# Kernel optimization log

Hardware: AMD Instinct MI355X
Metric: run time of the kernel (lower is better)

## Reference

```python
import jax, jax.numpy as jnp
import numpy as np

N, E, C, NB, NE, G = 20000, 320000, 64, 8, 4, 16
L2 = 9          # (max_ell+1)^2 with max_ell=2
RMAX = 5.0
HID = 16        # nonlinear readout hidden width


def setup_inputs():
    key = jax.random.key(0)
    ks = jax.random.split(key, 16)
    positions = jax.random.uniform(ks[0], (N, 3), dtype=jnp.float32) * 3.0
    elems = jax.random.randint(ks[1], (N,), 0, NE)
    node_attrs = jax.nn.one_hot(elems, NE, dtype=jnp.float32)
    edge_index = jax.random.randint(ks[2], (2, E), 0, N)
    batch = jnp.sort(jax.random.randint(ks[3], (N,), 0, G))
    shifts = jnp.zeros((E, 3), jnp.float32)
    atomic_energies = jnp.array([-1.0, -2.0, -3.0, -4.0], jnp.float32)
    sc = lambda k, shp, fan: jax.random.normal(k, shp, jnp.float32) / np.sqrt(fan).astype(np.float32)
    W_embed = sc(ks[4], (NE, C), NE)
    W_up = sc(ks[5], (2, C, C), C)
    W1 = sc(ks[6], (2, NB, 64), NB)
    W2 = sc(ks[7], (2, 64, C), 64)
    W_out = sc(ks[8], (2, C, C), C)
    W_skip = sc(ks[9], (2, NE, C), NE)
    w_read0 = sc(ks[10], (C,), C)
    W_r1 = sc(ks[11], (C, HID), C)
    w_r2 = sc(ks[12], (HID,), HID)
    return dict(positions=positions, node_attrs=node_attrs, shifts=shifts,
                atomic_energies=atomic_energies, W_embed=W_embed, W_up=W_up,
                W1=W1, W2=W2, W_out=W_out, W_skip=W_skip, w_read0=w_read0,
                W_r1=W_r1, w_r2=w_r2, edge_index=edge_index, batch=batch)


def _sph_harm_l2(u):
    # component-normalized real spherical harmonics up to l=2 on unit vectors
    x, y, z = u[:, 0], u[:, 1], u[:, 2]
    s3, s5, s15 = jnp.sqrt(3.0), jnp.sqrt(5.0), jnp.sqrt(15.0)
    return jnp.stack([jnp.ones_like(x),
                      s3 * x, s3 * y, s3 * z,
                      s15 * x * y, s15 * y * z, 0.5 * s5 * (3.0 * z * z - 1.0),
                      s15 * x * z, 0.5 * s15 * (x * x - y * y)], axis=-1)


def _radial(r):
    # Bessel radial basis with polynomial cutoff (p=6)
    n = jnp.arange(1, NB + 1, dtype=jnp.float32)
    rb = jnp.sqrt(2.0 / RMAX) * jnp.sin(n * jnp.pi * r[:, None] / RMAX) / r[:, None]
    u = r / RMAX
    fc = 1.0 - 28.0 * u**6 + 48.0 * u**7 - 21.0 * u**8
    fc = jnp.where(u < 1.0, fc, 0.0)
    return rb * fc[:, None]


def _energy_contributions(positions, node_attrs, shifts, atomic_energies,
                          W_embed, W_up, W1, W2, W_out, W_skip,
                          w_read0, W_r1, w_r2, edge_index, batch):
    snd, rcv = edge_index[0], edge_index[1]
    vec = positions[snd] - positions[rcv] + shifts                  # [E,3]
    r = jnp.sqrt(jnp.sum(vec * vec, axis=-1) + 1e-12)               # [E]
    Y = _sph_harm_l2(vec / r[:, None])                              # [E,L2]
    ef = _radial(r)                                                 # [E,NB]
    # E0: per-element reference energies, summed per graph
    e0 = jax.ops.segment_sum(node_attrs @ atomic_energies, batch, num_segments=G)
    h0 = node_attrs @ W_embed                                       # [N,C] scalar feats
    h = jnp.zeros((positions.shape[0], L2, C), h0.dtype).at[:, 0, :].set(h0)
    readouts = [lambda s: s @ w_read0,
                lambda s: jax.nn.silu(s @ W_r1) @ w_r2]             # linear / nonlinear
    energies = [e0]
    for i in range(2):
        hu = jnp.einsum('nlc,cd->nld', h, W_up[i])                  # channel mix
        R = jax.nn.silu(ef @ W1[i]) @ W2[i]                         # radial MLP [E,C]
        s = jnp.einsum('elc,el->ec', hu[snd], Y)                    # equivariant contraction
        m = Y[:, :, None] * (R * s)[:, None, :]                     # [E,L2,C] messages
        agg = jax.ops.segment_sum(m, rcv, num_segments=positions.shape[0])
        h = jnp.einsum('nlc,cd->nld', agg, W_out[i])
        h = h.at[:, 0, :].add(node_attrs @ W_skip[i])               # scalar skip connection
        node_en = readouts[i](h[:, 0, :])                           # [N]
        energies.append(jax.ops.segment_sum(node_en, batch, num_segments=G))
    return jnp.stack(energies, axis=-1)                             # [G, num_interactions+1]


def reference(positions, node_attrs, shifts, atomic_energies, W_embed, W_up,
              W1, W2, W_out, W_skip, w_read0, W_r1, w_r2, edge_index, batch):
    contributions = _energy_contributions(positions, node_attrs, shifts,
        atomic_energies, W_embed, W_up, W1, W2, W_out, W_skip,
        w_read0, W_r1, w_r2, edge_index, batch)
    total_energy = jnp.sum(contributions, axis=-1)                  # [G]
    forces = -jax.grad(lambda p: jnp.sum(_energy_contributions(p, node_attrs,
        shifts, atomic_energies, W_embed, W_up, W1, W2, W_out, W_skip,
        w_read0, W_r1, w_r2, edge_index, batch)))(positions)        # [N,3]
    return total_energy, contributions, forces
```

## Files before the change

### kernel.cpp

```cpp
#include <hip/hip_runtime.h>
#include <cmath>

constexpr int N_  = 20000;
constexpr int E_  = 320000;
constexpr int NE_ = 4;
constexpr int G_  = 16;
constexpr int CAP = 96;
constexpr int TAB = 4096;
constexpr float RMAXF = 5.0f;
constexpr float PI_F  = 3.14159265358979323846f;
constexpr float S3  = 1.7320508075688772f;
constexpr float S5  = 2.2360679774997896f;
constexpr float S15 = 3.8729833462074170f;
constexpr float KC_ = 0.6324555320336759f;

typedef unsigned short u16;
typedef unsigned int   u32;
typedef _Float16 f16;
typedef _Float16 f16x2 __attribute__((ext_vector_type(2)));

#define DEV static __device__ __forceinline__

__device__ float g_fallback[110000000];

DEV float sigmoidf_(float x){ return 1.0f/(1.0f+__expf(-x)); }

DEV float b2f(u16 u){ return __uint_as_float(((u32)u)<<16); }
DEV u16  f2b(float f){
  u32 x = __float_as_uint(f);
  return (u16)((x + 0x7FFFu + ((x>>16)&1u)) >> 16);
}
DEV u16  f2h(float f){ union{f16 h; u16 u;} v; v.h=(f16)f; return v.u; }
DEV float h2f(u16 u){ union{u16 u2; f16 h;} v; v.u2=u; return (float)v.h; }

DEV f16x2 u2h(u32 x){ union{u32 u; f16x2 h;} v; v.u=x; return v.h; }
DEV u32 h2u(f16x2 h){ union{u32 u; f16x2 h;} v; v.h=h; return v.u; }
DEV u32 pkh(float a, float b){ f16x2 h; h.x=(f16)a; h.y=(f16)b; return h2u(h); }

DEV void ld4(const float* __restrict__ p, float* d){
  float4 a = ((const float4*)p)[0];
  d[0]=a.x; d[1]=a.y; d[2]=a.z; d[3]=a.w;
}
DEV void ld4b(const u16* __restrict__ p, float* d){
  ushort4 a = *(const ushort4*)p;
  d[0]=b2f(a.x); d[1]=b2f(a.y); d[2]=b2f(a.z); d[3]=b2f(a.w);
}
DEV void st8h(u16* p, const float* d){
  uint4 v;
  v.x = pkh(d[0],d[1]); v.y = pkh(d[2],d[3]);
  v.z = pkh(d[4],d[5]); v.w = pkh(d[6],d[7]);
  *(uint4*)p = v;
}

DEV float tlerp(const u16* __restrict__ tab, int i0, float f, int idx){
  return h2f(tab[i0*256+idx])*(1.0f-f) + h2f(tab[(i0+1)*256+idx])*f;
}

__global__ void k_cnt(const int* __restrict__ ei, int* __restrict__ cntR){
  int e = blockIdx.x*256 + threadIdx.x;
  atomicAdd(&cntR[ei[E_+e]], 1);
}

__global__ void k_scan(const int* __restrict__ cntR, int* __restrict__ offR){
  __shared__ int part[256];
  int t = threadIdx.x;
  constexpr int CH = (N_+255)/256;
  int base = t*CH;
  int s=0;
  for (int i=0;i<CH;++i){ int idx=base+i; if(idx<N_) s+=cntR[idx]; }
  part[t]=s; __syncthreads();
  for (int d=1; d<256; d<<=1){
    int v = (t>=d)? part[t-d] : 0;
    __syncthreads();
    part[t]+=v;
    __syncthreads();
  }
  int run = (t==0)?0:part[t-1];
  for (int i=0;i<CH;++i){ int idx=base+i; if(idx<N_){ offR[idx]=run; run+=cntR[idx]; } }
  if (t==255) offR[N_]=run;
}

__global__ void k_perm(const int* __restrict__ ei, const int* __restrict__ offR,
                       int* __restrict__ cntR2, int* __restrict__ cntS,
                       int* __restrict__ pe, int* __restrict__ pSnd, int* __restrict__ pRcv,
                       int* __restrict__ listS){
  int e = blockIdx.x*256 + threadIdx.x;
  int s = ei[e], r = ei[E_+e];
  int p = offR[r] + atomicAdd(&cntR2[r], 1);
  pe[p] = e; pSnd[p] = s; pRcv[p] = r;
  int q = atomicAdd(&cntS[s], 1); if (q < CAP) listS[s*CAP+q] = p;
}

__global__ void k_pre(const float* __restrict__ Wout0, const float* __restrict__ Wup1,
                      const float* __restrict__ Wskip0, const float* __restrict__ wread0,
                      float* __restrict__ WA, float* __restrict__ sa,
                      float* __restrict__ va, float* __restrict__ sv){
  int t = threadIdx.x;
  for (int idx=t; idx<4096; idx+=256){
    int c = idx>>6, d = idx&63;
    float acc=0.f;
    for (int m=0;m<64;++m) acc += Wout0[c*64+m]*Wup1[m*64+d];
    WA[idx]=acc;
  }
  {
    int k = t>>6, d = t&63;
    float acc=0.f;
    for (int m=0;m<64;++m) acc += Wskip0[k*64+m]*Wup1[m*64+d];
    sa[t]=acc;
  }
  if (t<64){
    float acc=0.f;
    for (int d=0;d<64;++d) acc += Wout0[t*64+d]*wread0[d];
    va[t]=acc;
  }
  if (t<4){
    float acc=0.f;
    for (int d=0;d<64;++d) acc += Wskip0[t*64+d]*wread0[d];
    sv[t]=acc;
  }
}

__global__ __launch_bounds__(256, 2)
void k_rtab(const float* __restrict__ W1g, const float* __restrict__ W2g,
            u16* __restrict__ tab){
  __shared__ float sW1[1024];
  __shared__ u32   sW2h[4096];
  __shared__ u32   sAh[32*36];
  int t = threadIdx.x;
  for (int i=t;i<1024;i+=256) sW1[i]=W1g[i];
  for (int i=t;i<4096;i+=256){
    int L = i>>11, rem = i&2047, kp = rem>>6, c = rem&63;
    sW2h[i] = pkh(W2g[L*4096 + (2*kp)*64 + c], W2g[L*4096 + (2*kp+1)*64 + c]);
  }
  __syncthreads();
  int wid=t>>6, lane=t&63, q=lane>>3, j=lane&7, c0=j*8;
  int slot = wid*8 + q;
  int knot = blockIdx.x*32 + slot;
  bool valid = (knot <= TAB);
  float rad = fmaxf((float)knot * (RMAXF/(float)TAB), 1e-6f);
  float inv = 1.0f/rad;
  float tt = rad*(1.0f/RMAXF);
  float fc = 0.0f, dfc = 0.0f;
  if (tt < 1.0f){
    float t2=tt*tt, t4=t2*t2, t5=t4*tt, t6=t5*tt, t7=t6*tt, t8=t7*tt;
    fc  = 1.0f - 28.0f*t6 + 48.0f*t7 - 21.0f*t8;
    dfc = (-168.0f*t5 + 336.0f*t6 - 168.0f*t7)*(1.0f/RMAXF);
  }
  float th = rad*(PI_F/RMAXF);
  float s1 = __sinf(th), c1 = __cosf(th);
  float base = KC_*inv*fc;
  float efv[8], gfv[8];
  {
    float sb = s1, cb = c1;
    #pragma unroll
    for (int b=0;b<8;++b){
      efv[b] = base*sb;
      float wb_ = (float)(b+1)*(PI_F/RMAXF);
      float rb  = KC_*sb*inv;
      float drb = KC_*(wb_*cb - sb*inv)*inv;
      gfv[b] = drb*fc + rb*dfc;
      float sn = sb*c1 + cb*s1;
      cb = cb*c1 - sb*s1;
      sb = sn;
    }
  }
  u32* myAh = sAh + slot*36;
  for (int L=0; L<2; ++L){
    const float* w1 = sW1 + L*512;
    const u32*  w2h = sW2h + L*2048;
    float zz[8]={0,0,0,0,0,0,0,0};
    float wgv[8]={0,0,0,0,0,0,0,0};
    #pragma unroll 4
    for (int b=0;b<8;++b){
      float efb = efv[b], gfb = gfv[b];
      const float4* w=(const float4*)(w1 + b*64 + c0);
      float4 wa=w[0], wb=w[1];
      zz[0]+=efb*wa.x; zz[1]+=efb*wa.y; zz[2]+=efb*wa.z; zz[3]+=efb*wa.w;
      zz[4]+=efb*wb.x; zz[5]+=efb*wb.y; zz[6]+=efb*wb.z; zz[7]+=efb*wb.w;
      wgv[0]+=gfb*wa.x; wgv[1]+=gfb*wa.y; wgv[2]+=gfb*wa.z; wgv[3]+=gfb*wa.w;
      wgv[4]+=gfb*wb.x; wgv[5]+=gfb*wb.y; wgv[6]+=gfb*wb.z; wgv[7]+=gfb*wb.w;
    }
    float a[8], dv[8];
    #pragma unroll
    for (int i=0;i<8;++i){
      float sg = sigmoidf_(zz[i]);
      a[i]  = zz[i]*sg;
      float sp = sg*(1.0f + zz[i]*(1.0f - sg));
      dv[i] = wgv[i]*sp;
    }
    {
      uint4 av;
      av.x = pkh(a[0],a[1]); av.y = pkh(a[2],a[3]);
      av.z = pkh(a[4],a[5]); av.w = pkh(a[6],a[7]);
      *(uint4*)(myAh + 4*j) = av;
    }
    {
      float r0=0.f,r1=0.f,r2=0.f,r3=0.f,r4=0.f,r5=0.f,r6=0.f,r7=0.f;
      #pragma unroll 2
      for (int kp4=0; kp4<8; ++kp4){
        uint4 dq = *(const uint4*)(myAh + 4*kp4);
        #pragma unroll
        for (int i=0;i<4;++i){
          u32 du = (i==0)?dq.x:(i==1)?dq.y:(i==2)?dq.z:dq.w;
          f16x2 dh = u2h(du);
          const u32* wrow = w2h + (4*kp4+i)*64 + c0;
          uint4 w0 = *(const uint4*)(wrow);
          uint4 w1v = *(const uint4*)(wrow+4);
          r0 = __builtin_amdgcn_fdot2(dh, u2h(w0.x),  r0, false);
          r1 = __builtin_amdgcn_fdot2(dh, u2h(w0.y),  r1, false);
          r2 = __builtin_amdgcn_fdot2(dh, u2h(w0.z),  r2, false);
          r3 = __builtin_amdgcn_fdot2(dh, u2h(w0.w),  r3, false);
          r4 = __builtin_amdgcn_fdot2(dh, u2h(w1v.x), r4, false);
          r5 = __builtin_amdgcn_fdot2(dh, u2h(w1v.y), r5, false);
          r6 = __builtin_amdgcn_fdot2(dh, u2h(w1v.z), r6, false);
          r7 = __builtin_amdgcn_fdot2(dh, u2h(w1v.w), r7, false);
        }
      }
      float racc[8] = {r0,r1,r2,r3,r4,r5,r6,r7};
      if (valid) st8h(tab + (size_t)knot*256 + L*64 + c0, racc);
    }
    {
      uint4 av;
      av.x = pkh(dv[0],dv[1]); av.y = pkh(dv[2],dv[3]);
      av.z = pkh(dv[4],dv[5]); av.w = pkh(dv[6],dv[7]);
      *(uint4*)(myAh + 4*j) = av;
    }
    {
      float r0=0.f,r1=0.f,r2=0.f,r3=0.f,r4=0.f,r5=0.f,r6=0.f,r7=0.f;
      #pragma unroll 2
      for (int kp4=0; kp4<8; ++kp4){
        uint4 dq = *(const uint4*)(myAh + 4*kp4);
        #pragma unroll
        for (int i=0;i<4;++i){
          u32 du = (i==0)?dq.x:(i==1)?dq.y:(i==2)?dq.z:dq.w;
          f16x2 dh = u2h(du);
          const u32* wrow = w2h + (4*kp4+i)*64 + c0;
          uint4 w0 = *(const uint4*)(wrow);
          uint4 w1v = *(const uint4*)(wrow+4);
          r0 = __builtin_amdgcn_fdot2(dh, u2h(w0.x),  r0, false);
          r1 = __builtin_amdgcn_fdot2(dh, u2h(w0.y),  r1, false);
          r2 = __builtin_amdgcn_fdot2(dh, u2h(w0.z),  r2, false);
          r3 = __builtin_amdgcn_fdot2(dh, u2h(w0.w),  r3, false);
          r4 = __builtin_amdgcn_fdot2(dh, u2h(w1v.x), r4, false);
          r5 = __builtin_amdgcn_fdot2(dh, u2h(w1v.y), r5, false);
          r6 = __builtin_amdgcn_fdot2(dh, u2h(w1v.z), r6, false);
          r7 = __builtin_amdgcn_fdot2(dh, u2h(w1v.w), r7, false);
        }
      }
      float qacc[8] = {r0,r1,r2,r3,r4,r5,r6,r7};
      if (valid) st8h(tab + (size_t)knot*256 + 128 + L*64 + c0, qacc);
    }
  }
}

__global__ void k_fwd_edge(const float* __restrict__ pos, const float* __restrict__ shifts,
                const int* __restrict__ pe, const int* __restrict__ pSnd,
                const int* __restrict__ pRcv,
                float* __restrict__ Y, float* __restrict__ u3,
                float* __restrict__ irr, float* __restrict__ xi){
  int e = blockIdx.x*256 + threadIdx.x;
  int eo  = pe[e];
  int snd = pSnd[e], rcv = pRcv[e];
  float vx = pos[snd*3+0]-pos[rcv*3+0]+shifts[(size_t)eo*3+0];
  float vy = pos[snd*3+1]-pos[rcv*3+1]+shifts[(size_t)eo*3+1];
  float vz = pos[snd*3+2]-pos[rcv*3+2]+shifts[(size_t)eo*3+2];
  float ss = vx*vx+vy*vy+vz*vz + 1e-12f;
  float rad = sqrtf(ss);
  float inv = 1.0f/rad;
  float x = vx*inv, y = vy*inv, z = vz*inv;
  irr[e]=inv;
  xi[e] = rad * ((float)TAB/RMAXF);
  u3[(size_t)e*3+0]=x; u3[(size_t)e*3+1]=y; u3[(size_t)e*3+2]=z;
  float* Ye = Y + (size_t)e*9;
  Ye[0]=1.0f;
  Ye[1]=S3*x; Ye[2]=S3*y; Ye[3]=S3*z;
  Ye[4]=S15*x*y; Ye[5]=S15*y*z;
  Ye[6]=0.5f*S5*(3.0f*z*z-1.0f);
  Ye[7]=S15*x*z;
  Ye[8]=0.5f*S15*(x*x-y*y);
}

__global__ void k_e0(const float* __restrict__ attrs, const float* __restrict__ ae,
                     const int* __restrict__ batch, float* __restrict__ out){
  __shared__ float bins[G_];
  int t = threadIdx.x;
  if (t < G_) bins[t] = 0.f;
  __syncthreads();
  int n = blockIdx.x*256 + t;
  if (n < N_){
    float v = 0.f;
    #pragma unroll
    for (int k=0;k<NE_;++k) v += attrs[n*NE_+k]*ae[k];
    atomicAdd(&bins[batch[n]], v);
  }
  __syncthreads();
  if (t < G_){
    float b = bins[t];
    if (b != 0.f){
      atomicAdd(&out[t], b);
      atomicAdd(&out[G_ + t*3 + 0], b);
    }
  }
}

__global__ void k_wembup(const float* __restrict__ Wemb, const float* __restrict__ Wup0,
                         float* __restrict__ WembUp){
  int t = threadIdx.x; int k = t>>6, c = t&63;
  float acc = 0.f;
  for (int j=0;j<64;++j) acc += Wemb[k*64+j]*Wup0[j*64+c];
  WembUp[k*64+c] = acc;
}

__global__ void k_hu0(const float* __restrict__ attrs, const float* __restrict__ WembUp,
                      float* __restrict__ hu0){
  int i = blockIdx.x*256 + threadIdx.x;
  int n = i>>6, c = i&63;
  float acc = 0.f;
  #pragma unroll
  for (int k=0;k<NE_;++k) acc += attrs[n*NE_+k]*WembUp[k*64+c];
  hu0[i] = acc;
}

__global__ void k_agg0(const int* __restrict__ offR, const int* __restrict__ pSnd,
                       const float* __restrict__ hu0,
                       const u16* __restrict__ tab, const float* __restrict__ xi,
                       const float* __restrict__ Y,
                       float* __restrict__ agg0){
  int t = threadIdx.x; int n = blockIdx.x*4 + (t>>6); int c = t&63;
  float acc[9] = {0,0,0,0,0,0,0,0,0};
  int p0 = offR[n], p1 = offR[n+1];
  for (int p=p0;p<p1;++p){
    int s = pSnd[p];
    float xiv = xi[p];
    float r0v = 0.f;
    if (xiv < (float)TAB){
      int i0 = (int)xiv; float f = xiv - (float)i0;
      r0v = tlerp(tab, i0, f, c);
    }
    float v = r0v*hu0[(size_t)s*64+c];
    #pragma unroll
    for (int l=0;l<9;++l) acc[l] += Y[(size_t)p*9+l]*v;
  }
  #pragma unroll
  for (int l=0;l<9;++l) agg0[((size_t)n*9+l)*64+c] = acc[l];
}

__global__ void k_s1(const int* __restrict__ cntS, const int* __restrict__ listS,
                     const u16* __restrict__ hu1, const float* __restrict__ Y,
                     u16* __restrict__ s1){
  int t = threadIdx.x; int n = blockIdx.x*4 + (t>>6); int c = t&63;
  float hu[9];
  #pragma unroll
  for (int l=0;l<9;++l) hu[l] = b2f(hu1[((size_t)n*9+l)*64+c]);
  int deg = min(cntS[n], CAP);
  #pragma unroll 2
  for (int j=0;j<deg;++j){
    int p = listS[n*CAP+j];
    float acc = 0.f;
    #pragma unroll
    for (int l=0;l<9;++l) acc += hu[l]*Y[(size_t)p*9+l];
    s1[(size_t)p*64+c] = f2h(acc);
  }
}

__global__ void k_agg1(const int* __restrict__ offR,
                       const u16* __restrict__ tab, const float* __restrict__ xi,
                       const u16* __restrict__ s1,
                       float* __restrict__ agg1){
  int t = threadIdx.x; int n = blockIdx.x*4 + (t>>6); int c = t&63;
  float acc = 0.f;
  int p0 = offR[n], p1 = offR[n+1];
  for (int p=p0;p<p1;++p){
    float xiv = xi[p];
    float r1v = 0.f;
    if (xiv < (float)TAB){
      int i0 = (int)xiv; float f = xiv - (float)i0;
      r1v = tlerp(tab, i0, f, 64 + c);
    }
    acc += r1v*h2f(s1[(size_t)p*64+c]);
  }
  agg1[(size_t)n*64+c] = acc;
}

__global__ void k_dhu1(const int* __restrict__ cntS, const int* __restrict__ listS,
                       const int* __restrict__ pRcv,
                       const u16* __restrict__ tab, const float* __restrict__ xi,
                       const float* __restrict__ ga1, const float* __restrict__ Y,
                       float* __restrict__ dhu1){
  int t = threadIdx.x; int n = blockIdx.x*4 + (t>>6); int c = t&63;
  float acc[9] = {0,0,0,0,0,0,0,0,0};
  int deg = min(cntS[n], CAP);
  #pragma unroll 2
  for (int j=0;j<deg;++j){
    int p = listS[n*CAP+j];
    int r = pRcv[p];
    float xiv = xi[p];
    float r1v = 0.f;
    if (xiv < (float)TAB){
      int i0 = (int)xiv; float f = xiv - (float)i0;
      r1v = tlerp(tab, i0, f, 64 + c);
    }
    float ds = r1v*ga1[(size_t)r*64+c];
    #pragma unroll
    for (int l=0;l<9;++l) acc[l] += Y[(size_t)p*9+l]*ds;
  }
  #pragma unroll
  for (int l=0;l<9;++l) dhu1[((size_t)n*9+l)*64+c] = acc[l];
}

template<bool TRANS, bool OUTB>
__global__ __launch_bounds__(256, 2)
void k_mm64(const float* __restrict__ in, const float* __restrict__ W,
            void* __restrict__ out, int rows, int lper,
            const float* __restrict__ attrs, const float* __restrict__ Wsk,
            const float* __restrict__ bias){
  __shared__ float sWT[64*68];
  __shared__ float sRow[4*68];
  int t = threadIdx.x;
  for (int i=t;i<4096;i+=256){
    int k=i&63, c=i>>6;
    sWT[c*68+k] = TRANS ? W[c*64+k] : W[k*64+c];
  }
  __syncthreads();
  int wid = t>>6, c = t&63;
  float wcol[64];
  {
    const float4* wp = (const float4*)(sWT + c*68);
    #pragma unroll
    for (int kk=0;kk<16;++kk){
      float4 w4 = wp[kk];
      wcol[4*kk+0]=w4.x; wcol[4*kk+1]=w4.y; wcol[4*kk+2]=w4.z; wcol[4*kk+3]=w4.w;
    }
  }
  float* myRow = sRow + wid*68;
  for (int it=0; it<8; ++it){
    int row = (blockIdx.x*8+it)*4 + wid;
    myRow[c] = in[(size_t)row*64+c];
    float acc = 0.f;
    #pragma unroll
    for (int kk=0;kk<16;++kk){
      float4 r4 = ((const float4*)myRow)[kk];
      acc += r4.x*wcol[4*kk+0] + r4.y*wcol[4*kk+1] + r4.z*wcol[4*kk+2] + r4.w*wcol[4*kk+3];
    }
    if (lper==1 || (row % 9)==0){
      int n = (lper==1) ? row : (row/9);
      if (attrs){
        #pragma unroll
        for (int k=0;k<NE_;++k) acc += attrs[n*NE_+k]*Wsk[k*64+c];
      }
      if (bias) acc += bias[c];
    }
    if (OUTB) ((u16*)out)[(size_t)row*64+c] = f2b(acc);
    else      ((float*)out)[(size_t)row*64+c] = acc;
  }
}

__global__ void k_read0(const float* __restrict__ agg0, const float* __restrict__ va,
                        const float* __restrict__ sv, const float* __restrict__ attrs,
                        const int* __restrict__ batch, float* __restrict__ out){
  __shared__ float bins[G_];
  int t = threadIdx.x;
  if (t < G_) bins[t] = 0.f;
  __syncthreads();
  int lane = t & 63, wid = t >> 6;
  int grp = lane >> 3, j = lane & 7;
  int n = blockIdx.x*32 + wid*8 + grp;
  const float* hp = agg0 + (size_t)n*576 + j*8;
  const float* wp = va + j*8;
  float4 h0 = ((const float4*)hp)[0], h4 = ((const float4*)hp)[1];
  float4 w0v = ((const float4*)wp)[0], w4v = ((const float4*)wp)[1];
  float v = h0.x*w0v.x + h0.y*w0v.y + h0.z*w0v.z + h0.w*w0v.w
          + h4.x*w4v.x + h4.y*w4v.y + h4.z*w4v.z + h4.w*w4v.w;
  v += __shfl_xor(v,1,64); v += __shfl_xor(v,2,64); v += __shfl_xor(v,4,64);
  if (j==0){
    v += attrs[n*NE_+0]*sv[0] + attrs[n*NE_+1]*sv[1]
       + attrs[n*NE_+2]*sv[2] + attrs[n*NE_+3]*sv[3];
    atomicAdd(&bins[batch[n]], v);
  }
  __syncthreads();
  if (t < G_){
    float b = bins[t];
    if (b != 0.f){
      atomicAdd(&out[t], b);
      atomicAdd(&out[G_ + t*3 + 1], b);
    }
  }
}

__global__ void k_read1(const float* __restrict__ h2, const float* __restrict__ Wr1,
                        const float* __restrict__ wr2, const int* __restrict__ batch,
                        float* __restrict__ spz, float* __restrict__ out){
  __shared__ float sW[64*16];
  __shared__ float sA[256];
  __shared__ float bins[G_];
  int t = threadIdx.x;
  for (int i=t;i<1024;i+=256) sW[i]=Wr1[i];
  if (t < G_) bins[t] = 0.f;
  __syncthreads();
  int n = blockIdx.x*16 + (t>>4); int j = t&15;
  float z = 0.f;
  #pragma unroll 16
  for (int c=0;c<64;++c) z += h2[(size_t)n*64+c]*sW[c*16+j];
  float sg = sigmoidf_(z);
  float a  = z*sg;
  float sp = sg*(1.0f + z*(1.0f - sg));
  float w2v = wr2[j];
  spz[n*16+j] = sp*w2v;
  sA[t] = a*w2v;
  __syncthreads();
  if (j==0){
    float s = 0.f;
    #pragma unroll
    for (int k=0;k<16;++k) s += sA[t+k];
    atomicAdd(&bins[batch[n]], s);
  }
  __syncthreads();
  if (t < G_){
    float b = bins[t];
    if (b != 0.f){
      atomicAdd(&out[t], b);
      atomicAdd(&out[G_ + t*3 + 2], b);
    }
  }
}

__global__ void k_dh2(const float* __restrict__ Wr1, const float* __restrict__ spz,
                      float* __restrict__ dh2){
  int i = blockIdx.x*256 + threadIdx.x;
  int n = i>>6, c = i&63;
  float acc = 0.f;
  #pragma unroll
  for (int j=0;j<16;++j) acc += Wr1[c*16+j]*spz[n*16+j];
  dh2[i] = acc;
}

__global__ __launch_bounds__(256, 4)
void k_bedge_all(const int* __restrict__ pSnd, const int* __restrict__ pRcv,
             const float* __restrict__ Y,
             const float* __restrict__ u3, const float* __restrict__ irr,
             const u16* __restrict__ tab, const float* __restrict__ xi,
             const float* __restrict__ ga1, const u16* __restrict__ ga0,
             const float* __restrict__ hu0, const u16* __restrict__ hu1,
             float* __restrict__ gF){
  int t = threadIdx.x;
  int wid=t>>6, lane=t&63, q=lane>>4, j=lane&15, c0=j*4;
  int slot = wid*4+q;
  int e = blockIdx.x*16 + slot;
  int snd = pSnd[e], rcv = pRcv[e];
  float Yl[9];
  #pragma unroll
  for (int l=0;l<9;++l) Yl[l] = Y[(size_t)e*9+l];
  ushort4 huv1[9];
  #pragma unroll
  for (int l=0;l<9;++l) huv1[l] = *(const ushort4*)(hu1 + ((size_t)snd*9 + l)*64 + c0);
  ushort4 gv0[9];
  #pragma unroll
  for (int l=0;l<9;++l) gv0[l] = *(const ushort4*)(ga0 + ((size_t)rcv*9 + l)*64 + c0);
  float T1[4];  ld4(ga1 + (size_t)rcv*64 + c0, T1);
  float hu0v[4]; ld4(hu0 + (size_t)snd*64 + c0, hu0v);
  float xiv = xi[e];
  float R0v[4], R1v[4], q0v[4], q1v[4];
  if (xiv < (float)TAB){
    int i0 = (int)xiv; float f = xiv - (float)i0, g = 1.0f - f;
    const u16* ra = tab + (size_t)i0*256;
    const u16* rb = ra + 256;
    ushort4 a, b;
    a = *(const ushort4*)(ra + c0);        b = *(const ushort4*)(rb + c0);
    R0v[0]=h2f(a.x)*g+h2f(b.x)*f; R0v[1]=h2f(a.y)*g+h2f(b.y)*f;
    R0v[2]=h2f(a.z)*g+h2f(b.z)*f; R0v[3]=h2f(a.w)*g+h2f(b.w)*f;
    a = *(const ushort4*)(ra + 64 + c0);   b = *(const ushort4*)(rb + 64 + c0);
    R1v[0]=h2f(a.x)*g+h2f(b.x)*f; R1v[1]=h2f(a.y)*g+h2f(b.y)*f;
    R1v[2]=h2f(a.z)*g+h2f(b.z)*f; R1v[3]=h2f(a.w)*g+h2f(b.w)*f;
    a = *(const ushort4*)(ra + 128 + c0);  b = *(const ushort4*)(rb + 128 + c0);
    q0v[0]=h2f(a.x)*g+h2f(b.x)*f; q0v[1]=h2f(a.y)*g+h2f(b.y)*f;
    q0v[2]=h2f(a.z)*g+h2f(b.z)*f; q0v[3]=h2f(a.w)*g+h2f(b.w)*f;
    a = *(const ushort4*)(ra + 192 + c0);  b = *(const ushort4*)(rb + 192 + c0);
    q1v[0]=h2f(a.x)*g+h2f(b.x)*f; q1v[1]=h2f(a.y)*g+h2f(b.y)*f;
    q1v[2]=h2f(a.z)*g+h2f(b.z)*f; q1v[3]=h2f(a.w)*g+h2f(b.w)*f;
  } else {
    #pragma unroll
    for (int i=0;i<4;++i){ R0v[i]=0.f; R1v[i]=0.f; q0v[i]=0.f; q1v[i]=0.f; }
  }
  float dyp[9];
  float dR1[4];
  {
    float ds1[4], sA[4];
    #pragma unroll
    for (int i=0;i<4;++i){ ds1[i]=R1v[i]*T1[i]; sA[i]=0.f; }
    #pragma unroll
    for (int l=0;l<9;++l){
      float h0v=b2f(huv1[l].x), h1v=b2f(huv1[l].y), h2v=b2f(huv1[l].z), h3v=b2f(huv1[l].w);
      float Ylv = Yl[l];
      sA[0]+=h0v*Ylv; sA[1]+=h1v*Ylv; sA[2]+=h2v*Ylv; sA[3]+=h3v*Ylv;
      dyp[l] = ds1[0]*h0v + ds1[1]*h1v + ds1[2]*h2v + ds1[3]*h3v;
    }
    #pragma unroll
    for (int i=0;i<4;++i) dR1[i]=sA[i]*T1[i];
  }
  float dR0[4];
  {
    float P[4], T0[4];
    #pragma unroll
    for (int i=0;i<4;++i){ P[i]=R0v[i]*hu0v[i]; T0[i]=0.f; }
    #pragma unroll
    for (int l=0;l<9;++l){
      float g0=b2f(gv0[l].x), g1=b2f(gv0[l].y), g2=b2f(gv0[l].z), g3=b2f(gv0[l].w);
      float Ylv = Yl[l];
      T0[0]+=g0*Ylv; T0[1]+=g1*Ylv; T0[2]+=g2*Ylv; T0[3]+=g3*Ylv;
      dyp[l] += g0*P[0] + g1*P[1] + g2*P[2] + g3*P[3];
    }
    #pragma unroll
    for (int i=0;i<4;++i) dR0[i]=hu0v[i]*T0[i];
  }
  float dy[9];
  #pragma unroll
  for (int l=1;l<9;++l){
    float v=dyp[l];
    v += __shfl_xor(v,1,64); v += __shfl_xor(v,2,64);
    v += __shfl_xor(v,4,64); v += __shfl_xor(v,8,64);
    dy[l]=v;
  }
  float dr = q1v[0]*dR1[0]+q1v[1]*dR1[1]+q1v[2]*dR1[2]+q1v[3]*dR1[3]
           + q0v[0]*dR0[0]+q0v[1]*dR0[1]+q0v[2]*dR0[2]+q0v[3]*dR0[3];
  dr += __shfl_xor(dr,1,64); dr += __shfl_xor(dr,2,64);
  dr += __shfl_xor(dr,4,64); dr += __shfl_xor(dr,8,64);
  float x = u3[(size_t)e*3+0], y = u3[(size_t)e*3+1], zz = u3[(size_t)e*3+2];
  float invr = irr[e];
  float dux = S3*dy[1] + S15*(y*dy[4] + zz*dy[7] + x*dy[8]);
  float duy = S3*dy[2] + S15*(x*dy[4] + zz*dy[5] - y*dy[8]);
  float duz = S3*dy[3] + S15*(y*dy[5] + x*dy[7]) + 3.0f*S5*zz*dy[6];
  float udot = x*dux + y*duy + zz*duz;
  float gx = dr*x + invr*(dux - x*udot);
  float gy = dr*y + invr*(duy - y*udot);
  float gz = dr*zz + invr*(duz - zz*udot);
  if (j==0){
    float* gp2 = gF + (size_t)e*3;
    gp2[0]=gx; gp2[1]=gy; gp2[2]=gz;
  }
}

__global__ void k_fsum(const int* __restrict__ offR, const int* __restrict__ cntS,
                       const int* __restrict__ listS,
                       const float* __restrict__ gF, float* __restrict__ F){
  int t = threadIdx.x;
  int lane = t & 63, wid = t >> 6;
  int sub = lane >> 3, j = lane & 7;
  int n = blockIdx.x*32 + wid*8 + sub;
  float fx=0.f, fy=0.f, fz=0.f;
  int p0 = offR[n], p1 = offR[n+1];
  for (int p=p0+j; p<p1; p+=8){
    fx += gF[(size_t)p*3+0]; fy += gF[(size_t)p*3+1]; fz += gF[(size_t)p*3+2];
  }
  int dSn = min(cntS[n], CAP);
  for (int k=j;k<dSn;k+=8){
    int p = listS[n*CAP+k];
    fx -= gF[(size_t)p*3+0]; fy -= gF[(size_t)p*3+1]; fz -= gF[(size_t)p*3+2];
  }
  fx += __shfl_xor(fx,1,64); fy += __shfl_xor(fy,1,64); fz += __shfl_xor(fz,1,64);
  fx += __shfl_xor(fx,2,64); fy += __shfl_xor(fy,2,64); fz += __shfl_xor(fz,2,64);
  fx += __shfl_xor(fx,4,64); fy += __shfl_xor(fy,4,64); fz += __shfl_xor(fz,4,64);
  if (j==0){
    F[n*3+0]=fx; F[n*3+1]=fy; F[n*3+2]=fz;
  }
}

extern "C" void kernel_launch(void* const* d_in, const int* in_sizes, int n_in,
                              void* d_out, int out_size, void* d_ws, size_t ws_size,
                              hipStream_t stream){
  (void)in_sizes; (void)n_in;
  const float* pos    = (const float*)d_in[0];
  const float* attrs  = (const float*)d_in[1];
  const float* shifts = (const float*)d_in[2];
  const float* ae     = (const float*)d_in[3];
  const float* Wemb   = (const float*)d_in[4];
  const float* Wup    = (const float*)d_in[5];
  const float* W1     = (const float*)d_in[6];
  const float* W2     = (const float*)d_in[7];
  const float* Wout   = (const float*)d_in[8];
  const float* Wskip  = (const float*)d_in[9];
  const float* wread0 = (const float*)d_in[10];
  const float* Wr1    = (const float*)d_in[11];
  const float* wr2    = (const float*)d_in[12];
  const int*   ei     = (const int*)d_in[13];
  const int*   batch  = (const int*)d_in[14];
  float* out = (float*)d_out;

  const size_t NEED = 430000000;
  char* base;
  if (ws_size >= NEED){
    base = (char*)d_ws;
  } else {
    void* p = nullptr;
    hipGetSymbolAddress(&p, HIP_SYMBOL(g_fallback));
    base = (char*)p;
  }
  size_t off = 0;
  auto alloc = [&](size_t bytes)->char*{
    char* p = base + off;
    off += ((bytes + 255)/256)*256;
    return p;
  };
  float* Y    = (float*)alloc((size_t)E_*9*4);
  float* u3   = (float*)alloc((size_t)E_*3*4);
  float* irr  = (float*)alloc((size_t)E_*4);
  float* xi   = (float*)alloc((size_t)E_*4);
  u16*   s1b  = (u16*)  alloc((size_t)E_*64*2);
  float* gF   = (float*)alloc((size_t)E_*3*4);
  u16*   tab  = (u16*)  alloc((size_t)(TAB+1)*256*2);
  float* hu0  = (float*)alloc((size_t)N_*64*4);
  u16*   hu1  = (u16*)  alloc((size_t)N_*9*64*2);
  float* agg0 = (float*)alloc((size_t)N_*9*64*4);
  float* agg1 = (float*)alloc((size_t)N_*64*4);
  float* h2   = (float*)alloc((size_t)N_*64*4);
  float* spz  = (float*)alloc((size_t)N_*16*4);
  float* dh2  = (float*)alloc((size_t)N_*64*4);
  float* ga1  = (float*)alloc((size_t)N_*64*4);
  u16*   ga0  = (u16*)  alloc((size_t)N_*9*64*2);
  float* WembUp = (float*)alloc(256*4);
  float* WA   = (float*)alloc(4096*4);
  float* sa   = (float*)alloc(256*4);
  float* va   = (float*)alloc(64*4);
  float* sv   = (float*)alloc(4*4);
  int* cnts  = (int*)alloc((size_t)3*N_*4);
  int* offR  = (int*)alloc((size_t)(N_+1)*4);
  int* pe    = (int*)alloc((size_t)E_*4);
  int* pSnd  = (int*)alloc((size_t)E_*4);
  int* pRcv  = (int*)alloc((size_t)E_*4);
  int* listS = (int*)alloc((size_t)N_*CAP*4);
  int* cntR = cnts;  int* cntS = cnts + N_;  int* cntR2 = cnts + 2*N_;
  float* dhu1 = agg0;
  float* F = out + G_ + G_*3;

  hipMemsetAsync(d_out, 0, (size_t)out_size*sizeof(float), stream);
  hipMemsetAsync(cnts, 0, (size_t)3*N_*sizeof(int), stream);

  k_cnt     <<<E_/256, 256, 0, stream>>>(ei, cntR);
  k_scan    <<<1, 256, 0, stream>>>(cntR, offR);
  k_perm    <<<E_/256, 256, 0, stream>>>(ei, offR, cntR2, cntS, pe, pSnd, pRcv, listS);

  k_rtab    <<<(TAB+1+31)/32, 256, 0, stream>>>(W1, W2, tab);
  k_fwd_edge<<<E_/256, 256, 0, stream>>>(pos, shifts, pe, pSnd, pRcv, Y, u3, irr, xi);
  k_wembup  <<<1, 256, 0, stream>>>(Wemb, Wup, WembUp);
  k_pre     <<<1, 256, 0, stream>>>(Wout, Wup + 4096, Wskip, wread0, WA, sa, va, sv);
  k_e0      <<<(N_+255)/256, 256, 0, stream>>>(attrs, ae, batch, out);
  k_hu0     <<<N_*64/256, 256, 0, stream>>>(attrs, WembUp, hu0);
  k_agg0    <<<N_/4, 256, 0, stream>>>(offR, pSnd, hu0, tab, xi, Y, agg0);
  k_mm64<false,true><<<N_*9/32, 256, 0, stream>>>(agg0, WA, hu1, N_*9, 9, attrs, sa, nullptr);
  k_read0   <<<N_/32, 256, 0, stream>>>(agg0, va, sv, attrs, batch, out);
  k_s1      <<<N_/4, 256, 0, stream>>>(cntS, listS, hu1, Y, s1b);
  k_agg1    <<<N_/4, 256, 0, stream>>>(offR, tab, xi, s1b, agg1);
  k_mm64<false,false><<<N_/32, 256, 0, stream>>>(agg1, Wout + 4096, h2, N_, 1, attrs, Wskip + 256, nullptr);
  k_read1   <<<N_/16, 256, 0, stream>>>(h2, Wr1, wr2, batch, spz, out);

  k_dh2     <<<N_*64/256, 256, 0, stream>>>(Wr1, spz, dh2);
  k_mm64<true,false><<<N_/32, 256, 0, stream>>>(dh2, Wout + 4096, ga1, N_, 1, nullptr, nullptr, nullptr);
  k_dhu1    <<<N_/4, 256, 0, stream>>>(cntS, listS, pRcv, tab, xi, ga1, Y, dhu1);
  k_mm64<true,true><<<N_*9/32, 256, 0, stream>>>(dhu1, WA, ga0, N_*9, 9, nullptr, nullptr, va);
  k_bedge_all<<<E_/16, 256, 0, stream>>>(pSnd, pRcv, Y, u3, irr, tab, xi, ga1, ga0, hu0, hu1, gF);
  k_fsum    <<<N_/32, 256, 0, stream>>>(offR, cntS, listS, gF, F);
}
```

Measured before the change: 762.6 us.

## Store spherical harmonics and node aggregates in fp16, drop constant Y0

Per-edge spherical harmonics are stored as 8 fp16 values instead of 9 fp32, since the l=0 term is always 1 and is now folded in directly. The agg0/dhu1 node buffers become fp16, and k_mm64 gains a template flag to read fp16 input. The WembUp precompute is merged into k_pre, removing one launch. The aim is to cut memory traffic in the edge and node gather kernels, at the cost of reduced precision in the aggregated features and their gradients.

After: 751.8 us. About the same (-1.4%).

```diff
diff --git a/kernel.cpp b/kernel.cpp
--- a/kernel.cpp
+++ b/kernel.cpp
@@ -51,6 +51,12 @@
   v.z = pkh(d[4],d[5]); v.w = pkh(d[6],d[7]);
   *(uint4*)p = v;
 }
+DEV void ldY(const u16* __restrict__ p, float* Yb){
+  ushort4 a = *(const ushort4*)p;
+  ushort4 b = *(const ushort4*)(p+4);
+  Yb[0]=h2f(a.x); Yb[1]=h2f(a.y); Yb[2]=h2f(a.z); Yb[3]=h2f(a.w);
+  Yb[4]=h2f(b.x); Yb[5]=h2f(b.y); Yb[6]=h2f(b.z); Yb[7]=h2f(b.w);
+}
 
 DEV float tlerp(const u16* __restrict__ tab, int i0, float f, int idx){
   return h2f(tab[i0*256+idx])*(1.0f-f) + h2f(tab[(i0+1)*256+idx])*f;
@@ -93,8 +99,10 @@
 
 __global__ void k_pre(const float* __restrict__ Wout0, const float* __restrict__ Wup1,
                       const float* __restrict__ Wskip0, const float* __restrict__ wread0,
+                      const float* __restrict__ Wemb, const float* __restrict__ Wup0,
                       float* __restrict__ WA, float* __restrict__ sa,
-                      float* __restrict__ va, float* __restrict__ sv){
+                      float* __restrict__ va, float* __restrict__ sv,
+                      float* __restrict__ WembUp){
   int t = threadIdx.x;
   for (int idx=t; idx<4096; idx+=256){
     int c = idx>>6, d = idx&63;
@@ -107,6 +115,9 @@
     float acc=0.f;
     for (int m=0;m<64;++m) acc += Wskip0[k*64+m]*Wup1[m*64+d];
     sa[t]=acc;
+    float acc2=0.f;
+    for (int j=0;j<64;++j) acc2 += Wemb[k*64+j]*Wup0[j*64+d];
+    WembUp[t]=acc2;
   }
   if (t<64){
     float acc=0.f;
@@ -256,7 +267,7 @@
 __global__ void k_fwd_edge(const float* __restrict__ pos, const float* __restrict__ shifts,
                 const int* __restrict__ pe, const int* __restrict__ pSnd,
                 const int* __restrict__ pRcv,
-                float* __restrict__ Y, float* __restrict__ u3,
+                u16* __restrict__ Y, float* __restrict__ u3,
                 float* __restrict__ irr, float* __restrict__ xi){
   int e = blockIdx.x*256 + threadIdx.x;
   int eo  = pe[e];
@@ -271,13 +282,13 @@
   irr[e]=inv;
   xi[e] = rad * ((float)TAB/RMAXF);
   u3[(size_t)e*3+0]=x; u3[(size_t)e*3+1]=y; u3[(size_t)e*3+2]=z;
-  float* Ye = Y + (size_t)e*9;
-  Ye[0]=1.0f;
-  Ye[1]=S3*x; Ye[2]=S3*y; Ye[3]=S3*z;
-  Ye[4]=S15*x*y; Ye[5]=S15*y*z;
-  Ye[6]=0.5f*S5*(3.0f*z*z-1.0f);
-  Ye[7]=S15*x*z;
-  Ye[8]=0.5f*S15*(x*x-y*y);
+  float Yf[8];
+  Yf[0]=S3*x; Yf[1]=S3*y; Yf[2]=S3*z;
+  Yf[3]=S15*x*y; Yf[4]=S15*y*z;
+  Yf[5]=0.5f*S5*(3.0f*z*z-1.0f);
+  Yf[6]=S15*x*z;
+  Yf[7]=0.5f*S15*(x*x-y*y);
+  st8h(Y + (size_t)e*8, Yf);
 }
 
 __global__ void k_e0(const float* __restrict__ attrs, const float* __restrict__ ae,
@@ -301,14 +312,6 @@
       atomicAdd(&out[G_ + t*3 + 0], b);
     }
   }
-}
-
-__global__ void k_wembup(const float* __restrict__ Wemb, const float* __restrict__ Wup0,
-                         float* __restrict__ WembUp){
-  int t = threadIdx.x; int k = t>>6, c = t&63;
-  float acc = 0.f;
-  for (int j=0;j<64;++j) acc += Wemb[k*64+j]*Wup0[j*64+c];
-  WembUp[k*64+c] = acc;
 }
 
 __global__ void k_hu0(const float* __restrict__ attrs, const float* __restrict__ WembUp,
@@ -324,8 +327,8 @@
 __global__ void k_agg0(const int* __restrict__ offR, const int* __restrict__ pSnd,
                        const float* __restrict__ hu0,
                        const u16* __restrict__ tab, const float* __restrict__ xi,
-                       const float* __restrict__ Y,
-                       float* __restrict__ agg0){
+                       const u16* __restrict__ Y,
+                       u16* __restrict__ agg0){
   int t = threadIdx.x; int n = blockIdx.x*4 + (t>>6); int c = t&63;
   float acc[9] = {0,0,0,0,0,0,0,0,0};
   int p0 = offR[n], p1 = offR[n+1];
@@ -338,15 +341,18 @@
       r0v = tlerp(tab, i0, f, c);
     }
     float v = r0v*hu0[(size_t)s*64+c];
-    #pragma unroll
-    for (int l=0;l<9;++l) acc[l] += Y[(size_t)p*9+l]*v;
+    float Yb[8];
+    ldY(Y + (size_t)p*8, Yb);
+    acc[0] += v;
+    #pragma unroll
+    for (int l=1;l<9;++l) acc[l] += Yb[l-1]*v;
   }
   #pragma unroll
-  for (int l=0;l<9;++l) agg0[((size_t)n*9+l)*64+c] = acc[l];
+  for (int l=0;l<9;++l) agg0[((size_t)n*9+l)*64+c] = f2h(acc[l]);
 }
 
 __global__ void k_s1(const int* __restrict__ cntS, const int* __restrict__ listS,
-                     const u16* __restrict__ hu1, const float* __restrict__ Y,
+                     const u16* __restrict__ hu1, const u16* __restrict__ Y,
                      u16* __restrict__ s1){
   int t = threadIdx.x; int n = blockIdx.x*4 + (t>>6); int c = t&63;
   float hu[9];
@@ -356,9 +362,11 @@
   #pragma unroll 2
   for (int j=0;j<deg;++j){
     int p = listS[n*CAP+j];
-    float acc = 0.f;
-    #pragma unroll
-    for (int l=0;l<9;++l) acc += hu[l]*Y[(size_t)p*9+l];
+    float Yb[8];
+    ldY(Y + (size_t)p*8, Yb);
+    float acc = hu[0];
+    #pragma unroll
+    for (int l=1;l<9;++l) acc += hu[l]*Yb[l-1];
     s1[(size_t)p*64+c] = f2h(acc);
   }
 }
@@ -385,8 +393,8 @@
 __global__ void k_dhu1(const int* __restrict__ cntS, const int* __restrict__ listS,
                        const int* __restrict__ pRcv,
                        const u16* __restrict__ tab, const float* __restrict__ xi,
-                       const float* __restrict__ ga1, const float* __restrict__ Y,
-                       float* __restrict__ dhu1){
+                       const float* __restrict__ ga1, const u16* __restrict__ Y,
+                       u16* __restrict__ dhu1){
   int t = threadIdx.x; int n = blockIdx.x*4 + (t>>6); int c = t&63;
   float acc[9] = {0,0,0,0,0,0,0,0,0};
   int deg = min(cntS[n], CAP);
@@ -401,16 +409,19 @@
       r1v = tlerp(tab, i0, f, 64 + c);
     }
     float ds = r1v*ga1[(size_t)r*64+c];
-    #pragma unroll
-    for (int l=0;l<9;++l) acc[l] += Y[(size_t)p*9+l]*ds;
+    float Yb[8];
+    ldY(Y + (size_t)p*8, Yb);
+    acc[0] += ds;
+    #pragma unroll
+    for (int l=1;l<9;++l) acc[l] += Yb[l-1]*ds;
   }
   #pragma unroll
-  for (int l=0;l<9;++l) dhu1[((size_t)n*9+l)*64+c] = acc[l];
-}
-
-template<bool TRANS, bool OUTB>
+  for (int l=0;l<9;++l) dhu1[((size_t)n*9+l)*64+c] = f2h(acc[l]);
+}
+
+template<bool TRANS, bool OUTB, bool IN16>
 __global__ __launch_bounds__(256, 2)
-void k_mm64(const float* __restrict__ in, const float* __restrict__ W,
+void k_mm64(const void* __restrict__ in, const float* __restrict__ W,
             void* __restrict__ out, int rows, int lper,
             const float* __restrict__ attrs, const float* __restrict__ Wsk,
             const float* __restrict__ bias){
@@ -435,7 +446,8 @@
   float* myRow = sRow + wid*68;
   for (int it=0; it<8; ++it){
     int row = (blockIdx.x*8+it)*4 + wid;
-    myRow[c] = in[(size_t)row*64+c];
+    if (IN16) myRow[c] = h2f(((const u16*)in)[(size_t)row*64+c]);
+    else      myRow[c] = ((const float*)in)[(size_t)row*64+c];
     float acc = 0.f;
     #pragma unroll
     for (int kk=0;kk<16;++kk){
@@ -455,7 +467,7 @@
   }
 }
 
-__global__ void k_read0(const float* __restrict__ agg0, const float* __restrict__ va,
+__global__ void k_read0(const u16* __restrict__ agg0, const float* __restrict__ va,
                         const float* __restrict__ sv, const float* __restrict__ attrs,
                         const int* __restrict__ batch, float* __restrict__ out){
   __shared__ float bins[G_];
@@ -465,12 +477,13 @@
   int lane = t & 63, wid = t >> 6;
   int grp = lane >> 3, j = lane & 7;
   int n = blockIdx.x*32 + wid*8 + grp;
-  const float* hp = agg0 + (size_t)n*576 + j*8;
+  const u16* hp = agg0 + (size_t)n*576 + j*8;
+  float h[8];
+  ldY(hp, h);
   const float* wp = va + j*8;
-  float4 h0 = ((const float4*)hp)[0], h4 = ((const float4*)hp)[1];
   float4 w0v = ((const float4*)wp)[0], w4v = ((const float4*)wp)[1];
-  float v = h0.x*w0v.x + h0.y*w0v.y + h0.z*w0v.z + h0.w*w0v.w
-          + h4.x*w4v.x + h4.y*w4v.y + h4.z*w4v.z + h4.w*w4v.w;
+  float v = h[0]*w0v.x + h[1]*w0v.y + h[2]*w0v.z + h[3]*w0v.w
+          + h[4]*w4v.x + h[5]*w4v.y + h[6]*w4v.z + h[7]*w4v.w;
   v += __shfl_xor(v,1,64); v += __shfl_xor(v,2,64); v += __shfl_xor(v,4,64);
   if (j==0){
     v += attrs[n*NE_+0]*sv[0] + attrs[n*NE_+1]*sv[1]
@@ -536,7 +549,7 @@
 
 __global__ __launch_bounds__(256, 4)
 void k_bedge_all(const int* __restrict__ pSnd, const int* __restrict__ pRcv,
-             const float* __restrict__ Y,
+             const u16* __restrict__ Y,
              const float* __restrict__ u3, const float* __restrict__ irr,
              const u16* __restrict__ tab, const float* __restrict__ xi,
              const float* __restrict__ ga1, const u16* __restrict__ ga0,
@@ -548,8 +561,8 @@
   int e = blockIdx.x*16 + slot;
   int snd = pSnd[e], rcv = pRcv[e];
   float Yl[9];
-  #pragma unroll
-  for (int l=0;l<9;++l) Yl[l] = Y[(size_t)e*9+l];
+  Yl[0]=1.0f;
+  ldY(Y + (size_t)e*8, Yl+1);
   ushort4 huv1[9];
   #pragma unroll
   for (int l=0;l<9;++l) huv1[l] = *(const ushort4*)(hu1 + ((size_t)snd*9 + l)*64 + c0);
@@ -700,7 +713,7 @@
     off += ((bytes + 255)/256)*256;
     return p;
   };
-  float* Y    = (float*)alloc((size_t)E_*9*4);
+  u16*   Y    = (u16*)  alloc((size_t)E_*8*2);
   float* u3   = (float*)alloc((size_t)E_*3*4);
   float* irr  = (float*)alloc((size_t)E_*4);
   float* xi   = (float*)alloc((size_t)E_*4);
@@ -709,7 +722,7 @@
   u16*   tab  = (u16*)  alloc((size_t)(TAB+1)*256*2);
   float* hu0  = (float*)alloc((size_t)N_*64*4);
   u16*   hu1  = (u16*)  alloc((size_t)N_*9*64*2);
-  float* agg0 = (float*)alloc((size_t)N_*9*64*4);
+  u16*   agg0 = (u16*)  alloc((size_t)N_*9*64*2);
   float* agg1 = (float*)alloc((size_t)N_*64*4);
   float* h2   = (float*)alloc((size_t)N_*64*4);
   float* spz  = (float*)alloc((size_t)N_*16*4);
@@ -728,7 +741,7 @@
   int* pRcv  = (int*)alloc((size_t)E_*4);
   int* listS = (int*)alloc((size_t)N_*CAP*4);
   int* cntR = cnts;  int* cntS = cnts + N_;  int* cntR2 = cnts + 2*N_;
-  float* dhu1 = agg0;
+  u16* dhu1 = agg0;
   float* F = out + G_ + G_*3;
 
   hipMemsetAsync(d_out, 0, (size_t)out_size*sizeof(float), stream);
@@ -740,22 +753,21 @@
 
   k_rtab    <<<(TAB+1+31)/32, 256, 0, stream>>>(W1, W2, tab);
   k_fwd_edge<<<E_/256, 256, 0, stream>>>(pos, shifts, pe, pSnd, pRcv, Y, u3, irr, xi);
-  k_wembup  <<<1, 256, 0, stream>>>(Wemb, Wup, WembUp);
-  k_pre     <<<1, 256, 0, stream>>>(Wout, Wup + 4096, Wskip, wread0, WA, sa, va, sv);
+  k_pre     <<<1, 256, 0, stream>>>(Wout, Wup + 4096, Wskip, wread0, Wemb, Wup, WA, sa, va, sv, WembUp);
   k_e0      <<<(N_+255)/256, 256, 0, stream>>>(attrs, ae, batch, out);
   k_hu0     <<<N_*64/256, 256, 0, stream>>>(attrs, WembUp, hu0);
   k_agg0    <<<N_/4, 256, 0, stream>>>(offR, pSnd, hu0, tab, xi, Y, agg0);
-  k_mm64<false,true><<<N_*9/32, 256, 0, stream>>>(agg0, WA, hu1, N_*9, 9, attrs, sa, nullptr);
+  k_mm64<false,true,true><<<N_*9/32, 256, 0, stream>>>(agg0, WA, hu1, N_*9, 9, attrs, sa, nullptr);
   k_read0   <<<N_/32, 256, 0, stream>>>(agg0, va, sv, attrs, batch, out);
   k_s1      <<<N_/4, 256, 0, stream>>>(cntS, listS, hu1, Y, s1b);
   k_agg1    <<<N_/4, 256, 0, stream>>>(offR, tab, xi, s1b, agg1);
-  k_mm64<false,false><<<N_/32, 256, 0, stream>>>(agg1, Wout + 4096, h2, N_, 1, attrs, Wskip + 256, nullptr);
+  k_mm64<false,false,false><<<N_/32, 256, 0, stream>>>(agg1, Wout + 4096, h2, N_, 1, attrs, Wskip + 256, nullptr);
   k_read1   <<<N_/16, 256, 0, stream>>>(h2, Wr1, wr2, batch, spz, out);
 
   k_dh2     <<<N_*64/256, 256, 0, stream>>>(Wr1, spz, dh2);
-  k_mm64<true,false><<<N_/32, 256, 0, stream>>>(dh2, Wout + 4096, ga1, N_, 1, nullptr, nullptr, nullptr);
+  k_mm64<true,false,false><<<N_/32, 256, 0, stream>>>(dh2, Wout + 4096, ga1, N_, 1, nullptr, nullptr, nullptr);
   k_dhu1    <<<N_/4, 256, 0, stream>>>(cntS, listS, pRcv, tab, xi, ga1, Y, dhu1);
-  k_mm64<true,true><<<N_*9/32, 256, 0, stream>>>(dhu1, WA, ga0, N_*9, 9, nullptr, nullptr, va);
+  k_mm64<true,true,true><<<N_*9/32, 256, 0, stream>>>(dhu1, WA, ga0, N_*9, 9, nullptr, nullptr, va);
   k_bedge_all<<<E_/16, 256, 0, stream>>>(pSnd, pRcv, Y, u3, irr, tab, xi, ga1, ga0, hu0, hu1, gF);
   k_fsum    <<<N_/32, 256, 0, stream>>>(offR, cntS, listS, gF, F);
 }
```
